# Optimization experiments

Measured on AMD Instinct MI355X. Metric: run time of the kernel, lower is better.

The kernel has to match this reference:

```python
import jax, jax.numpy as jnp
import numpy as np

H = 4       # N_head
C = 32      # c_hidden
CZ = 128    # c_z
N = 256
B = 1
EPS = 1e-5


def setup_inputs() -> dict:
    key = jax.random.key(0)
    ks = jax.random.split(key, 8)
    hc = H * C
    return {
        "z": jax.random.normal(ks[0], (B, N, N, CZ), dtype=jnp.float32),
        "ln_scale": jnp.ones((CZ,), dtype=jnp.float32),
        "ln_bias": jnp.zeros((CZ,), dtype=jnp.float32),
        "Wq": jax.random.normal(ks[1], (CZ, hc), dtype=jnp.float32) * 0.02,
        "Wk": jax.random.normal(ks[2], (CZ, hc), dtype=jnp.float32) * 0.02,
        "Wv": jax.random.normal(ks[3], (CZ, hc), dtype=jnp.float32) * 0.02,
        "Wb": jax.random.normal(ks[4], (CZ, H), dtype=jnp.float32) * 0.02,
        "Wg": jax.random.normal(ks[5], (CZ, hc), dtype=jnp.float32) * 0.02,
        "Wo": jax.random.normal(ks[6], (hc, CZ), dtype=jnp.float32) * 0.02,
    }


def reference(z, ln_scale, ln_bias, Wq, Wk, Wv, Wb, Wg, Wo):
    b, n = z.shape[0], z.shape[1]
    # LayerNorm over c_z
    mu = jnp.mean(z, axis=-1, keepdims=True)
    var = jnp.mean(jnp.square(z - mu), axis=-1, keepdims=True)
    zn = (z - mu) * jax.lax.rsqrt(var + EPS) * ln_scale + ln_bias
    # projections -> [B, N, N, H, C]
    q = (zn @ Wq).reshape(b, n, n, H, C)
    k = (zn @ Wk).reshape(b, n, n, H, C)
    v = (zn @ Wv).reshape(b, n, n, H, C)
    bias = zn @ Wb                                  # [B, N, N, H]
    g = jax.nn.sigmoid(zn @ Wg).reshape(b, n, n, H, C)
    # attention around starting node i: query at (i,j), keys/values at (i,k)
    scores = jnp.einsum('bijhd,bikhd->bijkh', q, k) * (1.0 / C ** 0.5)
    scores = scores + bias[:, None, :, :, :]        # bias[b, j, k, h]
    a = jax.nn.softmax(scores, axis=-2)             # softmax over k
    o = jnp.einsum('bijkh,bikhd->bijhd', a, v)      # [B, N, N, H, C]
    o = (g * o).reshape(b, n, n, H * C)
    return o @ Wo
```

## Files before the change

### kernel.cpp

```cpp
#include <hip/hip_runtime.h>
#include <math.h>

#define NN 256
#define CZ 128
#define NH 4
#define CH 32
#define HC 128
#define NPIX (NN*NN)
#define SCALE 0.17677669529663687f
#define L2E   1.4426950408889634f
#define SCALE2 (0.17677669529663687f * 1.4426950408889634f)

typedef __attribute__((ext_vector_type(8))) short bf16x8;
typedef __attribute__((ext_vector_type(4))) float fx4;

__device__ __forceinline__ unsigned short f2bf(float f) {
    unsigned u = __builtin_bit_cast(unsigned, f);
    u += 0x7FFFu + ((u >> 16) & 1u);
    return (unsigned short)(u >> 16);
}
__device__ __forceinline__ float bf2f(unsigned short s) {
    return __builtin_bit_cast(float, (unsigned)s << 16);
}
__device__ __forceinline__ void load_split8(const float* p, bf16x8& h, bf16x8& l) {
    float4 x0 = *(const float4*)p;
    float4 x1 = *(const float4*)(p + 4);
    float xs[8] = {x0.x, x0.y, x0.z, x0.w, x1.x, x1.y, x1.z, x1.w};
    #pragma unroll
    for (int j = 0; j < 8; ++j) {
        unsigned short hs = f2bf(xs[j]);
        h[j] = (short)hs;
        l[j] = (short)f2bf(xs[j] - bf2f(hs));
    }
}

__global__ __launch_bounds__(256) void pack_w_kernel(
    const float* __restrict__ Wq, const float* __restrict__ Wk,
    const float* __restrict__ Wv, const float* __restrict__ Wg,
    const float* __restrict__ Wo, bf16x8* __restrict__ pk)
{
    int id  = blockIdx.x * 256 + threadIdx.x;
    int mid = id >> 11;
    int e   = id & 2047;
    const float* W = (mid == 0) ? Wq : (mid == 1) ? Wk : (mid == 2) ? Wv : (mid == 3) ? Wg : Wo;
    int quad = e & 3, n = (e >> 2) & 127, ks = e >> 9;
    int k0 = ks * 32 + quad * 8;
    bf16x8 h, l;
    #pragma unroll
    for (int j = 0; j < 8; ++j) {
        float x = W[(size_t)(k0 + j) * 128 + n];
        unsigned short hs = f2bf(x);
        h[j] = (short)hs;
        l[j] = (short)f2bf(x - bf2f(hs));
    }
    pk[(size_t)mid * 4096 + e]        = h;
    pk[(size_t)mid * 4096 + 2048 + e] = l;
}

__global__ __launch_bounds__(256) void ln_proj_kernel(
    const float* __restrict__ z, const float* __restrict__ ls, const float* __restrict__ lb,
    const float* __restrict__ Wb, const bf16x8* __restrict__ pk,
    float* __restrict__ q_ws, float* __restrict__ k_ws, float* __restrict__ v_t,
    float* __restrict__ g_ws, float* __restrict__ bias_t)
{
    __shared__ float zsh[32][132];
    __shared__ float rsum[256], rsq[256];
    __shared__ float pmu[32], prs[32];

    const int t  = threadIdx.x;
    const int p0 = blockIdx.x * 32;
    const int i  = p0 >> 8;
    const int j0 = p0 & 255;

    const float4* z4 = (const float4*)(z + (size_t)p0 * CZ);
    #pragma unroll
    for (int r = 0; r < 4; ++r) {
        int idx4 = t + 256 * r;
        int p = idx4 >> 5, pos = idx4 & 31;
        *(float4*)&zsh[p][pos * 4] = z4[idx4];
    }
    __syncthreads();

    {
        int p = t >> 3, sg = t & 7;
        float s = 0.f, q = 0.f;
        #pragma unroll
        for (int u = 0; u < 16; ++u) { float x = zsh[p][sg * 16 + u]; s += x; q += x * x; }
        rsum[t] = s; rsq[t] = q;
    }
    __syncthreads();
    if (t < 32) {
        float s = 0.f, q = 0.f;
        #pragma unroll
        for (int g = 0; g < 8; ++g) { s += rsum[t * 8 + g]; q += rsq[t * 8 + g]; }
        float mu  = s * (1.0f / 128.0f);
        float var = q * (1.0f / 128.0f) - mu * mu;
        float a   = var + 1e-5f;
        float r   = rsqrtf(a);
        r = r * (1.5f - 0.5f * a * r * r);
        pmu[t] = mu; prs[t] = r;
    }
    __syncthreads();

    #pragma unroll
    for (int r4 = 0; r4 < 4; ++r4) {
        int idx4 = t + 256 * r4;
        int p = idx4 >> 5, pos = idx4 & 31;
        float4 v  = *(float4*)&zsh[p][pos * 4];
        float4 s4 = ((const float4*)ls)[pos];
        float4 b4 = ((const float4*)lb)[pos];
        float mu = pmu[p], rs = prs[p];
        v.x = (v.x - mu) * rs * s4.x + b4.x;
        v.y = (v.y - mu) * rs * s4.y + b4.y;
        v.z = (v.z - mu) * rs * s4.z + b4.z;
        v.w = (v.w - mu) * rs * s4.w + b4.w;
        *(float4*)&zsh[p][pos * 4] = v;
    }
    __syncthreads();

    const int wv = t >> 6, lane = t & 63;
    const int lrow = lane & 15, quad = lane >> 4;
    const bf16x8* ph = pk + (size_t)wv * 4096;
    const bf16x8* pl = ph + 2048;

    fx4 acc[2][8];
    #pragma unroll
    for (int mr = 0; mr < 2; ++mr)
        #pragma unroll
        for (int nc = 0; nc < 8; ++nc)
            acc[mr][nc] = fx4{0.f, 0.f, 0.f, 0.f};

    #pragma unroll
    for (int ks = 0; ks < 4; ++ks) {
        bf16x8 ah[2], al[2];
        #pragma unroll
        for (int mr = 0; mr < 2; ++mr)
            load_split8(&zsh[mr * 16 + lrow][ks * 32 + quad * 8], ah[mr], al[mr]);
        #pragma unroll
        for (int nc = 0; nc < 8; ++nc) {
            int bi = (ks * 128 + nc * 16 + lrow) * 4 + quad;
            bf16x8 bh = ph[bi], bl = pl[bi];
            #pragma unroll
            for (int mr = 0; mr < 2; ++mr) {
                acc[mr][nc] = __builtin_amdgcn_mfma_f32_16x16x32_bf16(ah[mr], bl, acc[mr][nc], 0, 0, 0);
                acc[mr][nc] = __builtin_amdgcn_mfma_f32_16x16x32_bf16(al[mr], bh, acc[mr][nc], 0, 0, 0);
                acc[mr][nc] = __builtin_amdgcn_mfma_f32_16x16x32_bf16(ah[mr], bh, acc[mr][nc], 0, 0, 0);
            }
        }
    }

    #pragma unroll
    for (int mr = 0; mr < 2; ++mr) {
        #pragma unroll
        for (int nc = 0; nc < 8; ++nc) {
            int cg = nc * 16 + lrow;
            int h = cg >> 5, cc = cg & 31;
            int jl = mr * 16 + quad * 4;
            fx4 a = acc[mr][nc];
            if (wv == 0) {
                float* qp = q_ws + ((size_t)(i * NH + h) * NN + j0 + jl) * CH + cc;
                #pragma unroll
                for (int r = 0; r < 4; ++r) qp[r * CH] = a[r];
            } else if (wv == 1) {
                float* kp = k_ws + ((size_t)(i * NH + h) * NN + j0 + jl) * CH + cc;
                #pragma unroll
                for (int r = 0; r < 4; ++r) kp[r * CH] = a[r];
            } else if (wv == 2) {
                float4 f = make_float4(a[0], a[1], a[2], a[3]);
                *(float4*)(v_t + ((size_t)(i * NH + h) * CH + cc) * NN + j0 + jl) = f;
            } else {
                float* gp = g_ws + (size_t)(p0 + jl) * HC + cg;
                #pragma unroll
                for (int r = 0; r < 4; ++r) gp[r * HC] = 1.0f / (1.0f + __expf(-a[r]));
            }
        }
    }

    if (t < 128) {
        int p = t >> 2, hh = t & 3;
        float b = 0.f;
        for (int d = 0; d < 128; ++d) b = fmaf(zsh[p][d], Wb[d * 4 + hh], b);
        bias_t[(size_t)hh * NPIX + (size_t)(j0 + p) * NN + i] = b * L2E;
    }
}

#define PSTR 40
__global__ __launch_bounds__(256) void attn_kernel(
    const float* __restrict__ q_ws, const float* __restrict__ k_ws,
    const float* __restrict__ v_t,  const float* __restrict__ g_ws,
    const float* __restrict__ bias_t, float* __restrict__ go_ws)
{
    __shared__ unsigned short Psh[4][2][64 * PSTR];

    const int t = threadIdx.x;
    const int wv = t >> 6, lane = t & 63;
    const int lrow = lane & 15, quad = lane >> 4;
    const int h = blockIdx.x & 3, i = blockIdx.x >> 2;
    const int qb = wv * 64;

    const float* qs = q_ws + (size_t)(i * NH + h) * NN * CH;
    const float* ks = k_ws + (size_t)(i * NH + h) * NN * CH;
    const float* vs = v_t  + (size_t)(i * NH + h) * CH * NN;
    const float* bs = bias_t + (size_t)h * NPIX;

    bf16x8 qh[4], ql[4];
    #pragma unroll
    for (int nt = 0; nt < 4; ++nt)
        load_split8(qs + (size_t)(qb + nt * 16 + lrow) * CH + quad * 8, qh[nt], ql[nt]);

    fx4 oacc[2][4];
    #pragma unroll
    for (int ct = 0; ct < 2; ++ct)
        #pragma unroll
        for (int nt = 0; nt < 4; ++nt)
            oacc[ct][nt] = fx4{0.f, 0.f, 0.f, 0.f};
    float lsum[4] = {0.f, 0.f, 0.f, 0.f};

    for (int kb = 0; kb < NN; kb += 32) {
        bf16x8 kh[2], kl_[2];
        #pragma unroll
        for (int mt = 0; mt < 2; ++mt)
            load_split8(ks + (size_t)(kb + mt * 16 + lrow) * CH + quad * 8, kh[mt], kl_[mt]);
        bf16x8 vh[2], vl[2];
        #pragma unroll
        for (int ct = 0; ct < 2; ++ct)
            load_split8(vs + (size_t)(ct * 16 + lrow) * NN + kb + quad * 8, vh[ct], vl[ct]);

        #pragma unroll
        for (int nt = 0; nt < 4; ++nt) {
            #pragma unroll
            for (int mt = 0; mt < 2; ++mt) {
                float bias_r[4];
                #pragma unroll
                for (int r = 0; r < 4; ++r)
                    bias_r[r] = bs[(size_t)(kb + mt * 16 + quad * 4 + r) * NN + qb + nt * 16 + lrow];

                fx4 sv = fx4{0.f, 0.f, 0.f, 0.f};
                sv = __builtin_amdgcn_mfma_f32_16x16x32_bf16(kh[mt], ql[nt], sv, 0, 0, 0);
                sv = __builtin_amdgcn_mfma_f32_16x16x32_bf16(kl_[mt], qh[nt], sv, 0, 0, 0);
                sv = __builtin_amdgcn_mfma_f32_16x16x32_bf16(kh[mt], qh[nt], sv, 0, 0, 0);

                unsigned short hs[4], lo[4];
                #pragma unroll
                for (int r = 0; r < 4; ++r) {
                    float e = exp2f(fmaf(sv[r], SCALE2, bias_r[r]));
                    lsum[nt] += e;
                    hs[r] = f2bf(e);
                    lo[r] = (unsigned short)f2bf(e - bf2f(hs[r]));
                }
                int wo = (nt * 16 + lrow) * PSTR + mt * 16 + quad * 4;
                *(uint2*)&Psh[wv][0][wo] =
                    make_uint2((unsigned)hs[0] | ((unsigned)hs[1] << 16),
                               (unsigned)hs[2] | ((unsigned)hs[3] << 16));
                *(uint2*)&Psh[wv][1][wo] =
                    make_uint2((unsigned)lo[0] | ((unsigned)lo[1] << 16),
                               (unsigned)lo[2] | ((unsigned)lo[3] << 16));
            }
        }

        #pragma unroll
        for (int nt = 0; nt < 4; ++nt) {
            bf16x8 pbh = *(const bf16x8*)&Psh[wv][0][(nt * 16 + lrow) * PSTR + quad * 8];
            bf16x8 pbl = *(const bf16x8*)&Psh[wv][1][(nt * 16 + lrow) * PSTR + quad * 8];
            #pragma unroll
            for (int ct = 0; ct < 2; ++ct) {
                oacc[ct][nt] = __builtin_amdgcn_mfma_f32_16x16x32_bf16(vh[ct], pbl, oacc[ct][nt], 0, 0, 0);
                oacc[ct][nt] = __builtin_amdgcn_mfma_f32_16x16x32_bf16(vl[ct], pbh, oacc[ct][nt], 0, 0, 0);
                oacc[ct][nt] = __builtin_amdgcn_mfma_f32_16x16x32_bf16(vh[ct], pbh, oacc[ct][nt], 0, 0, 0);
            }
        }
    }

    #pragma unroll
    for (int nt = 0; nt < 4; ++nt) {
        float s = lsum[nt];
        s += __shfl_xor(s, 16, 64);
        s += __shfl_xor(s, 32, 64);
        float inv = 1.0f / s;
        size_t pix = (size_t)i * NN + qb + nt * 16 + lrow;
        #pragma unroll
        for (int ct = 0; ct < 2; ++ct) {
            const float* gp = g_ws + pix * HC + h * CH + ct * 16 + quad * 4;
            float4 g4 = *(const float4*)gp;
            fx4 o = oacc[ct][nt];
            float4 r;
            r.x = g4.x * o[0] * inv;
            r.y = g4.y * o[1] * inv;
            r.z = g4.z * o[2] * inv;
            r.w = g4.w * o[3] * inv;
            *(float4*)(go_ws + pix * HC + h * CH + ct * 16 + quad * 4) = r;
        }
    }
}

__global__ __launch_bounds__(256) void outproj_kernel(
    const float* __restrict__ go_ws, const bf16x8* __restrict__ pk, float* __restrict__ out)
{
    __shared__ float gsh[64][132];
    const int t  = threadIdx.x;
    const int p0 = blockIdx.x * 64;

    const float4* g4 = (const float4*)(go_ws + (size_t)p0 * HC);
    #pragma unroll
    for (int r = 0; r < 8; ++r) {
        int idx4 = t + 256 * r;
        int p = idx4 >> 5, pos = idx4 & 31;
        *(float4*)&gsh[p][pos * 4] = g4[idx4];
    }
    __syncthreads();

    const int wv = t >> 6, lane = t & 63;
    const int lrow = lane & 15, quad = lane >> 4;
    const bf16x8* ph = pk + (size_t)4 * 4096;
    const bf16x8* pl = ph + 2048;

    fx4 acc[8];
    #pragma unroll
    for (int nc = 0; nc < 8; ++nc) acc[nc] = fx4{0.f, 0.f, 0.f, 0.f};

    #pragma unroll
    for (int ks = 0; ks < 4; ++ks) {
        bf16x8 ah, al;
        load_split8(&gsh[wv * 16 + lrow][ks * 32 + quad * 8], ah, al);
        #pragma unroll
        for (int nc = 0; nc < 8; ++nc) {
            int bi = (ks * 128 + nc * 16 + lrow) * 4 + quad;
            bf16x8 bh = ph[bi], bl = pl[bi];
            acc[nc] = __builtin_amdgcn_mfma_f32_16x16x32_bf16(ah, bl, acc[nc], 0, 0, 0);
            acc[nc] = __builtin_amdgcn_mfma_f32_16x16x32_bf16(al, bh, acc[nc], 0, 0, 0);
            acc[nc] = __builtin_amdgcn_mfma_f32_16x16x32_bf16(ah, bh, acc[nc], 0, 0, 0);
        }
    }

    #pragma unroll
    for (int nc = 0; nc < 8; ++nc) {
        #pragma unroll
        for (int r = 0; r < 4; ++r)
            out[(size_t)(p0 + wv * 16 + quad * 4 + r) * HC + nc * 16 + lrow] = acc[nc][r];
    }
}

extern "C" void kernel_launch(void* const* d_in, const int* in_sizes, int n_in,
                              void* d_out, int out_size, void* d_ws, size_t ws_size,
                              hipStream_t stream)
{
    const float* z  = (const float*)d_in[0];
    const float* ls = (const float*)d_in[1];
    const float* lb = (const float*)d_in[2];
    const float* Wq = (const float*)d_in[3];
    const float* Wk = (const float*)d_in[4];
    const float* Wv = (const float*)d_in[5];
    const float* Wb = (const float*)d_in[6];
    const float* Wg = (const float*)d_in[7];
    const float* Wo = (const float*)d_in[8];

    float* ws = (float*)d_ws;
    const size_t BIG = (size_t)NPIX * HC;
    float* q_ws   = ws;
    float* k_ws   = ws + BIG;
    float* v_t    = ws + 2 * BIG;
    float* g_ws   = ws + 3 * BIG;
    float* go_ws  = ws + 4 * BIG;
    float* bias_t = ws + 5 * BIG;
    bf16x8* pk    = (bf16x8*)(bias_t + (size_t)NH * NPIX);

    pack_w_kernel<<<40, 256, 0, stream>>>(Wq, Wk, Wv, Wg, Wo, pk);
    ln_proj_kernel<<<NPIX / 32, 256, 0, stream>>>(z, ls, lb, Wb, pk,
                                                  q_ws, k_ws, v_t, g_ws, bias_t);
    attn_kernel<<<NN * NH, 256, 0, stream>>>(q_ws, k_ws, v_t, g_ws, bias_t, go_ws);
    outproj_kernel<<<NPIX / 64, 256, 0, stream>>>(go_ws, pk, (float*)d_out);
}
```

Baseline: 259.9 us.

## Pre-split Q/K/V into packed bf16 hi/lo words and store bias untransposed

The projection kernel now writes Q, K and V as packed 32-bit words holding the bf16 high and residual-low halves, so the attention kernel only deinterleaves instead of recomputing the split on every reload. The bias is stored in [h][i][j] order so attention can fetch four contiguous values with one float4 load rather than four strided scalar loads. Rounding for the bf16 split changes from round-to-nearest to truncation of the high part, which shifts the error slightly but keeps the three-term hi/lo product.

Result: faster. 247.3 us (-4.8%).

```diff
diff --git a/kernel.cpp b/kernel.cpp
--- a/kernel.cpp
+++ b/kernel.cpp
@@ -7,20 +7,18 @@
 #define CH 32
 #define HC 128
 #define NPIX (NN*NN)
-#define SCALE 0.17677669529663687f
 #define L2E   1.4426950408889634f
 #define SCALE2 (0.17677669529663687f * 1.4426950408889634f)
 
 typedef __attribute__((ext_vector_type(8))) short bf16x8;
 typedef __attribute__((ext_vector_type(4))) float fx4;
-
-__device__ __forceinline__ unsigned short f2bf(float f) {
-    unsigned u = __builtin_bit_cast(unsigned, f);
-    u += 0x7FFFu + ((u >> 16) & 1u);
-    return (unsigned short)(u >> 16);
-}
-__device__ __forceinline__ float bf2f(unsigned short s) {
-    return __builtin_bit_cast(float, (unsigned)s << 16);
+typedef __attribute__((ext_vector_type(4))) unsigned u32x4;
+
+__device__ __forceinline__ unsigned pack_hl(float x) {
+    unsigned b  = __builtin_bit_cast(unsigned, x);
+    unsigned hb = b & 0xFFFF0000u;
+    float r = x - __builtin_bit_cast(float, hb);
+    return hb | (__builtin_bit_cast(unsigned, r) >> 16);
 }
 __device__ __forceinline__ void load_split8(const float* p, bf16x8& h, bf16x8& l) {
     float4 x0 = *(const float4*)p;
@@ -28,10 +26,26 @@
     float xs[8] = {x0.x, x0.y, x0.z, x0.w, x1.x, x1.y, x1.z, x1.w};
     #pragma unroll
     for (int j = 0; j < 8; ++j) {
-        unsigned short hs = f2bf(xs[j]);
-        h[j] = (short)hs;
-        l[j] = (short)f2bf(xs[j] - bf2f(hs));
-    }
+        unsigned b  = __builtin_bit_cast(unsigned, xs[j]);
+        unsigned hb = b & 0xFFFF0000u;
+        float r = xs[j] - __builtin_bit_cast(float, hb);
+        h[j] = (short)(hb >> 16);
+        l[j] = (short)(__builtin_bit_cast(unsigned, r) >> 16);
+    }
+}
+__device__ __forceinline__ void deint8(const unsigned* p, bf16x8& h, bf16x8& l) {
+    u32x4 e0 = *(const u32x4*)p;
+    u32x4 e1 = *(const u32x4*)(p + 4);
+    unsigned es[8] = {e0[0], e0[1], e0[2], e0[3], e1[0], e1[1], e1[2], e1[3]};
+    unsigned hw[4], lw[4];
+    #pragma unroll
+    for (int j = 0; j < 4; ++j) {
+        unsigned a = es[2 * j], b = es[2 * j + 1];
+        hw[j] = (a >> 16) | (b & 0xFFFF0000u);
+        lw[j] = (a & 0x0000FFFFu) | (b << 16);
+    }
+    h = __builtin_bit_cast(bf16x8, u32x4{hw[0], hw[1], hw[2], hw[3]});
+    l = __builtin_bit_cast(bf16x8, u32x4{lw[0], lw[1], lw[2], lw[3]});
 }
 
 __global__ __launch_bounds__(256) void pack_w_kernel(
@@ -49,9 +63,11 @@
     #pragma unroll
     for (int j = 0; j < 8; ++j) {
         float x = W[(size_t)(k0 + j) * 128 + n];
-        unsigned short hs = f2bf(x);
-        h[j] = (short)hs;
-        l[j] = (short)f2bf(x - bf2f(hs));
+        unsigned b  = __builtin_bit_cast(unsigned, x);
+        unsigned hb = b & 0xFFFF0000u;
+        float r = x - __builtin_bit_cast(float, hb);
+        h[j] = (short)(hb >> 16);
+        l[j] = (short)(__builtin_bit_cast(unsigned, r) >> 16);
     }
     pk[(size_t)mid * 4096 + e]        = h;
     pk[(size_t)mid * 4096 + 2048 + e] = l;
@@ -60,8 +76,8 @@
 __global__ __launch_bounds__(256) void ln_proj_kernel(
     const float* __restrict__ z, const float* __restrict__ ls, const float* __restrict__ lb,
     const float* __restrict__ Wb, const bf16x8* __restrict__ pk,
-    float* __restrict__ q_ws, float* __restrict__ k_ws, float* __restrict__ v_t,
-    float* __restrict__ g_ws, float* __restrict__ bias_t)
+    unsigned* __restrict__ q_pk, unsigned* __restrict__ k_pk, unsigned* __restrict__ v_pk,
+    float* __restrict__ g_ws, float* __restrict__ bias_n)
 {
     __shared__ float zsh[32][132];
     __shared__ float rsum[256], rsq[256];
@@ -158,16 +174,16 @@
             int jl = mr * 16 + quad * 4;
             fx4 a = acc[mr][nc];
             if (wv == 0) {
-                float* qp = q_ws + ((size_t)(i * NH + h) * NN + j0 + jl) * CH + cc;
+                unsigned* qp = q_pk + ((size_t)(i * NH + h) * NN + j0 + jl) * CH + cc;
                 #pragma unroll
-                for (int r = 0; r < 4; ++r) qp[r * CH] = a[r];
+                for (int r = 0; r < 4; ++r) qp[r * CH] = pack_hl(a[r]);
             } else if (wv == 1) {
-                float* kp = k_ws + ((size_t)(i * NH + h) * NN + j0 + jl) * CH + cc;
+                unsigned* kp = k_pk + ((size_t)(i * NH + h) * NN + j0 + jl) * CH + cc;
                 #pragma unroll
-                for (int r = 0; r < 4; ++r) kp[r * CH] = a[r];
+                for (int r = 0; r < 4; ++r) kp[r * CH] = pack_hl(a[r]);
             } else if (wv == 2) {
-                float4 f = make_float4(a[0], a[1], a[2], a[3]);
-                *(float4*)(v_t + ((size_t)(i * NH + h) * CH + cc) * NN + j0 + jl) = f;
+                u32x4 e = {pack_hl(a[0]), pack_hl(a[1]), pack_hl(a[2]), pack_hl(a[3])};
+                *(u32x4*)(v_pk + ((size_t)(i * NH + h) * CH + cc) * NN + j0 + jl) = e;
             } else {
                 float* gp = g_ws + (size_t)(p0 + jl) * HC + cg;
                 #pragma unroll
@@ -177,18 +193,18 @@
     }
 
     if (t < 128) {
-        int p = t >> 2, hh = t & 3;
+        int hh = t >> 5, p = t & 31;
         float b = 0.f;
         for (int d = 0; d < 128; ++d) b = fmaf(zsh[p][d], Wb[d * 4 + hh], b);
-        bias_t[(size_t)hh * NPIX + (size_t)(j0 + p) * NN + i] = b * L2E;
+        bias_n[(size_t)hh * NPIX + (size_t)i * NN + j0 + p] = b * L2E;
     }
 }
 
 #define PSTR 40
 __global__ __launch_bounds__(256) void attn_kernel(
-    const float* __restrict__ q_ws, const float* __restrict__ k_ws,
-    const float* __restrict__ v_t,  const float* __restrict__ g_ws,
-    const float* __restrict__ bias_t, float* __restrict__ go_ws)
+    const unsigned* __restrict__ q_pk, const unsigned* __restrict__ k_pk,
+    const unsigned* __restrict__ v_pk, const float* __restrict__ g_ws,
+    const float* __restrict__ bias_n, float* __restrict__ go_ws)
 {
     __shared__ unsigned short Psh[4][2][64 * PSTR];
 
@@ -198,15 +214,15 @@
     const int h = blockIdx.x & 3, i = blockIdx.x >> 2;
     const int qb = wv * 64;
 
-    const float* qs = q_ws + (size_t)(i * NH + h) * NN * CH;
-    const float* ks = k_ws + (size_t)(i * NH + h) * NN * CH;
-    const float* vs = v_t  + (size_t)(i * NH + h) * CH * NN;
-    const float* bs = bias_t + (size_t)h * NPIX;
+    const unsigned* qs = q_pk + (size_t)(i * NH + h) * NN * CH;
+    const unsigned* ks = k_pk + (size_t)(i * NH + h) * NN * CH;
+    const unsigned* vs = v_pk + (size_t)(i * NH + h) * CH * NN;
+    const float*    bs = bias_n + (size_t)h * NPIX;
 
     bf16x8 qh[4], ql[4];
     #pragma unroll
     for (int nt = 0; nt < 4; ++nt)
-        load_split8(qs + (size_t)(qb + nt * 16 + lrow) * CH + quad * 8, qh[nt], ql[nt]);
+        deint8(qs + (size_t)(qb + nt * 16 + lrow) * CH + quad * 8, qh[nt], ql[nt]);
 
     fx4 oacc[2][4];
     #pragma unroll
@@ -220,41 +236,48 @@
         bf16x8 kh[2], kl_[2];
         #pragma unroll
         for (int mt = 0; mt < 2; ++mt)
-            load_split8(ks + (size_t)(kb + mt * 16 + lrow) * CH + quad * 8, kh[mt], kl_[mt]);
+            deint8(ks + (size_t)(kb + mt * 16 + lrow) * CH + quad * 8, kh[mt], kl_[mt]);
         bf16x8 vh[2], vl[2];
         #pragma unroll
         for (int ct = 0; ct < 2; ++ct)
-            load_split8(vs + (size_t)(ct * 16 + lrow) * NN + kb + quad * 8, vh[ct], vl[ct]);
+            deint8(vs + (size_t)(ct * 16 + lrow) * NN + kb + quad * 8, vh[ct], vl[ct]);
 
         #pragma unroll
         for (int nt = 0; nt < 4; ++nt) {
             #pragma unroll
             for (int mt = 0; mt < 2; ++mt) {
-                float bias_r[4];
-                #pragma unroll
-                for (int r = 0; r < 4; ++r)
-                    bias_r[r] = bs[(size_t)(kb + mt * 16 + quad * 4 + r) * NN + qb + nt * 16 + lrow];
+                float4 bv = *(const float4*)(bs + (size_t)(qb + nt * 16 + lrow) * NN
+                                                + kb + mt * 16 + quad * 4);
 
                 fx4 sv = fx4{0.f, 0.f, 0.f, 0.f};
                 sv = __builtin_amdgcn_mfma_f32_16x16x32_bf16(kh[mt], ql[nt], sv, 0, 0, 0);
                 sv = __builtin_amdgcn_mfma_f32_16x16x32_bf16(kl_[mt], qh[nt], sv, 0, 0, 0);
                 sv = __builtin_amdgcn_mfma_f32_16x16x32_bf16(kh[mt], qh[nt], sv, 0, 0, 0);
 
-                unsigned short hs[4], lo[4];
-                #pragma unroll
-                for (int r = 0; r < 4; ++r) {
-                    float e = exp2f(fmaf(sv[r], SCALE2, bias_r[r]));
-                    lsum[nt] += e;
-                    hs[r] = f2bf(e);
-                    lo[r] = (unsigned short)f2bf(e - bf2f(hs[r]));
-                }
+                float e0 = exp2f(fmaf(sv[0], SCALE2, bv.x));
+                float e1 = exp2f(fmaf(sv[1], SCALE2, bv.y));
+                float e2 = exp2f(fmaf(sv[2], SCALE2, bv.z));
+                float e3 = exp2f(fmaf(sv[3], SCALE2, bv.w));
+                lsum[nt] += (e0 + e1) + (e2 + e3);
+
+                unsigned b0 = __builtin_bit_cast(unsigned, e0);
+                unsigned b1 = __builtin_bit_cast(unsigned, e1);
+                unsigned b2 = __builtin_bit_cast(unsigned, e2);
+                unsigned b3 = __builtin_bit_cast(unsigned, e3);
+                unsigned h01 = (b0 >> 16) | (b1 & 0xFFFF0000u);
+                unsigned h23 = (b2 >> 16) | (b3 & 0xFFFF0000u);
+                float r0 = e0 - __builtin_bit_cast(float, b0 & 0xFFFF0000u);
+                float r1 = e1 - __builtin_bit_cast(float, b1 & 0xFFFF0000u);
+                float r2 = e2 - __builtin_bit_cast(float, b2 & 0xFFFF0000u);
+                float r3 = e3 - __builtin_bit_cast(float, b3 & 0xFFFF0000u);
+                unsigned l01 = (__builtin_bit_cast(unsigned, r0) >> 16)
+                             | (__builtin_bit_cast(unsigned, r1) & 0xFFFF0000u);
+                unsigned l23 = (__builtin_bit_cast(unsigned, r2) >> 16)
+                             | (__builtin_bit_cast(unsigned, r3) & 0xFFFF0000u);
+
                 int wo = (nt * 16 + lrow) * PSTR + mt * 16 + quad * 4;
-                *(uint2*)&Psh[wv][0][wo] =
-                    make_uint2((unsigned)hs[0] | ((unsigned)hs[1] << 16),
-                               (unsigned)hs[2] | ((unsigned)hs[3] << 16));
-                *(uint2*)&Psh[wv][1][wo] =
-                    make_uint2((unsigned)lo[0] | ((unsigned)lo[1] << 16),
-                               (unsigned)lo[2] | ((unsigned)lo[3] << 16));
+                *(uint2*)&Psh[wv][0][wo] = make_uint2(h01, h23);
+                *(uint2*)&Psh[wv][1][wo] = make_uint2(l01, l23);
             }
         }
 
@@ -356,17 +379,17 @@
 
     float* ws = (float*)d_ws;
     const size_t BIG = (size_t)NPIX * HC;
-    float* q_ws   = ws;
-    float* k_ws   = ws + BIG;
-    float* v_t    = ws + 2 * BIG;
-    float* g_ws   = ws + 3 * BIG;
-    float* go_ws  = ws + 4 * BIG;
-    float* bias_t = ws + 5 * BIG;
-    bf16x8* pk    = (bf16x8*)(bias_t + (size_t)NH * NPIX);
+    unsigned* q_pk  = (unsigned*)ws;
+    unsigned* k_pk  = (unsigned*)(ws + BIG);
+    unsigned* v_pk  = (unsigned*)(ws + 2 * BIG);
+    float* g_ws     = ws + 3 * BIG;
+    float* go_ws    = ws + 4 * BIG;
+    float* bias_n   = ws + 5 * BIG;
+    bf16x8* pk      = (bf16x8*)(bias_n + (size_t)NH * NPIX);
 
     pack_w_kernel<<<40, 256, 0, stream>>>(Wq, Wk, Wv, Wg, Wo, pk);
     ln_proj_kernel<<<NPIX / 32, 256, 0, stream>>>(z, ls, lb, Wb, pk,
-                                                  q_ws, k_ws, v_t, g_ws, bias_t);
-    attn_kernel<<<NN * NH, 256, 0, stream>>>(q_ws, k_ws, v_t, g_ws, bias_t, go_ws);
+                                                  q_pk, k_pk, v_pk, g_ws, bias_n);
+    attn_kernel<<<NN * NH, 256, 0, stream>>>(q_pk, k_pk, v_pk, g_ws, bias_n, go_ws);
     outproj_kernel<<<NPIX / 64, 256, 0, stream>>>(go_ws, pk, (float*)d_out);
 }
```
